# Kernel optimization log

Measured on AMD Instinct MI355X. Metric: run time of the kernel, lower is better.

## Reference

```python
import jax, jax.numpy as jnp
import numpy as np

B, D, R = 16384, 4096, 64       # batch tokens, embed_dim, low_rank_dimension
N_PART = 8                       # number of subspace partitions
P = R // N_PART                  # partition size = 8
N_SEL = 4                        # partitions selected per example


def setup_inputs() -> dict:
    key = jax.random.key(0)
    k1, k2, k3, k4 = jax.random.split(key, 4)
    base = jax.random.normal(k1, (B, D), dtype=jnp.float32)
    source = jax.random.normal(k2, (B, D), dtype=jnp.float32)
    # orthogonal low-rank rotation (torch.nn.utils.parametrizations.orthogonal)
    W, _ = jnp.linalg.qr(jax.random.normal(k3, (D, R), dtype=jnp.float32))  # [D, R], orthonormal cols
    subspaces = jax.random.randint(k4, (B, N_SEL), 0, N_PART)               # partition ids per example
    return {"base": base, "source": source, "W": W, "subspaces": subspaces}


def reference(base, source, W, subspaces):
    # rotate into low-rank space: [B, R]
    rotated_base = base @ W
    rotated_source = source @ W
    diff = rotated_source - rotated_base

    # per-example selected rotated-space indices (contiguous partitions of size P)
    # idx[b] = concat over selected partitions of [p*P, p*P+P)
    idx = (subspaces[:, :, None] * P + jnp.arange(P)).reshape(B, N_SEL * P)  # [B, N_SEL*P]

    # Selecting columns of diff and matching rows of W.T, then matmul, is
    # equivalent to masking unselected rotated dims to zero and doing one GEMM.
    mask = jnp.zeros((B, R), dtype=diff.dtype).at[jnp.arange(B)[:, None], idx].set(1.0)
    output = base + (diff * mask) @ W.T  # [B, D]
    return output.astype(base.dtype)
```

## Files before the change

kernel.cpp:

```cpp
#include <hip/hip_runtime.h>


#define D_DIM 4096
#define R_DIM 64
#define BM    32
#define WAVESTG 16384
#define OFF_RM  65536
#define SMEM_BYTES 70144

typedef short bf16vec8 __attribute__((ext_vector_type(8)));
typedef float f32x4v  __attribute__((ext_vector_type(4)));

#define VMWAIT(N)                                              \
  do {                                                         \
    asm volatile("s_waitcnt vmcnt(" #N ")" ::: "memory");      \
    __builtin_amdgcn_sched_barrier(0);                         \
  } while (0)

__device__ __forceinline__ unsigned int f2bf_u(float f) {
  unsigned int u = __builtin_bit_cast(unsigned int, f);
  return (u + 0x7fffu + ((u >> 16) & 1u)) >> 16;
}
__device__ __forceinline__ unsigned int pack2bf(float a, float b) {
  return f2bf_u(a) | (f2bf_u(b) << 16);
}
__device__ __forceinline__ void async_ld16(const void* g, void* l) {
  __builtin_amdgcn_global_load_lds(
      (const __attribute__((address_space(1))) void*)g,
      (__attribute__((address_space(3))) void*)l, 16, 0, 0);
}

__global__ __launch_bounds__(256)
void lrri_prep(const float* __restrict__ W, unsigned short* __restrict__ Wt,
               unsigned short* __restrict__ Wb) {
  const int idx = blockIdx.x * blockDim.x + threadIdx.x;
  const int k = idx >> 4;
  const int j = (idx & 15) * 4;
  float4 w = *(const float4*)(W + (size_t)k * R_DIM + j);
  ushort4 p;
  p.x = (unsigned short)f2bf_u(w.x);
  p.y = (unsigned short)f2bf_u(w.y);
  p.z = (unsigned short)f2bf_u(w.z);
  p.w = (unsigned short)f2bf_u(w.w);
  *(ushort4*)(Wb + (size_t)k * R_DIM + j) = p;
  Wt[(size_t)(j + 0) * D_DIM + k] = p.x;
  Wt[(size_t)(j + 1) * D_DIM + k] = p.y;
  Wt[(size_t)(j + 2) * D_DIM + k] = p.z;
  Wt[(size_t)(j + 3) * D_DIM + k] = p.w;
}

template<bool USE_WS>
__global__ __launch_bounds__(256, 2)
void lrri_fused(const float* __restrict__ base, const float* __restrict__ srcp,
                const float* __restrict__ W, const int* __restrict__ subs,
                const unsigned short* __restrict__ Wt_bf,
                const unsigned short* __restrict__ Wb_bf,
                float* __restrict__ out)
{
  __shared__ __align__(16) unsigned char smem[SMEM_BYTES];
  const int tid  = threadIdx.x;
  const int wave = tid >> 6;
  const int lane = tid & 63;
  const int l4   = lane & 15;
  const int g    = lane >> 4;
  const int rh   = wave >> 1;
  const int kh   = wave & 1;
  const long rowbase = (long)blockIdx.x * BM;
  const long rowg    = rowbase + rh * 16;
  unsigned char* wbuf = smem + wave * WAVESTG;
  const int off1 = (blockIdx.x * 7) & 63;
  const int off2 = (blockIdx.x * 5) & 15;

  f32x4v acc[4];
  #pragma unroll
  for (int t = 0; t < 4; ++t) acc[t] = (f32x4v){0.f, 0.f, 0.f, 0.f};

  auto stage = [&](int c) {
    const int ch = (c + off1) & 63;
    unsigned char* buf = wbuf + (c & 1) * 8192;
    const long colf = kh * 2048 + ch * 32;
    #pragma unroll
    for (int q = 0; q < 2; ++q) {
      const int r = q * 8 + (lane >> 3);
      const unsigned b = ((unsigned)((lane & 7) * 16)) ^ ((unsigned)(r & 7) << 4);
      const long goff = (rowg + r) * (long)D_DIM + colf + (b >> 2);
      async_ld16(base + goff, buf + q * 1024);
    }
    #pragma unroll
    for (int q = 0; q < 2; ++q) {
      const int r = q * 8 + (lane >> 3);
      const unsigned b = ((unsigned)((lane & 7) * 16)) ^ ((unsigned)(r & 7) << 4);
      const long goff = (rowg + r) * (long)D_DIM + colf + (b >> 2);
      async_ld16(srcp + goff, buf + 2048 + q * 1024);
    }
    #pragma unroll
    for (int q = 0; q < 4; ++q) {
      const int j = q * 16 + (lane >> 2);
      const unsigned kb = ((unsigned)((lane & 3) * 16)) ^ ((unsigned)(j & 3) << 4);
      const char* src = (const char*)Wt_bf + (size_t)j * (D_DIM * 2) +
                        colf * 2 + kb;
      async_ld16(src, buf + 4096 + q * 1024);
    }
  };

  auto compute = [&](int c) {
    const unsigned char* buf = wbuf + (c & 1) * 8192;
    const unsigned sw = (unsigned)((l4 & 7) << 4);
    const unsigned c0 = ((unsigned)(g * 32)) ^ sw;
    const unsigned c1 = ((unsigned)(g * 32 + 16)) ^ sw;
    float4 fb0 = *(const float4*)(buf + l4 * 128 + c0);
    float4 fb1 = *(const float4*)(buf + l4 * 128 + c1);
    float4 fs0 = *(const float4*)(buf + 2048 + l4 * 128 + c0);
    float4 fs1 = *(const float4*)(buf + 2048 + l4 * 128 + c1);
    uint4 af;
    af.x = pack2bf(fs0.x - fb0.x, fs0.y - fb0.y);
    af.y = pack2bf(fs0.z - fb0.z, fs0.w - fb0.w);
    af.z = pack2bf(fs1.x - fb1.x, fs1.y - fb1.y);
    af.w = pack2bf(fs1.z - fb1.z, fs1.w - fb1.w);
    const unsigned wsl = ((unsigned)(g * 16)) ^ ((unsigned)(l4 & 3) << 4);
    #pragma unroll
    for (int t = 0; t < 4; ++t) {
      uint4 wf = *(const uint4*)(buf + 4096 + (t * 16 + l4) * 64 + wsl);
      acc[t] = __builtin_amdgcn_mfma_f32_16x16x32_bf16(
          __builtin_bit_cast(bf16vec8, af),
          __builtin_bit_cast(bf16vec8, wf), acc[t], 0, 0, 0);
    }
  };

  if constexpr (USE_WS) {
    stage(0); stage(1);
    #pragma unroll 1
    for (int c = 0; c < 62; ++c) {
      VMWAIT(8);
      compute(c);
      __builtin_amdgcn_sched_barrier(0);
      stage(c + 2);
    }
    VMWAIT(8);
    compute(62);
    VMWAIT(0);
    compute(63);
  } else {
    #pragma unroll 1
    for (int c = 0; c < 64; ++c) {
      const int ch = (c + off1) & 63;
      unsigned char* buf = wbuf + (c & 1) * 8192;
      const long colf = kh * 2048 + ch * 32;
      #pragma unroll
      for (int q = 0; q < 2; ++q) {
        const int r = q * 8 + (lane >> 3);
        const unsigned b = ((unsigned)((lane & 7) * 16)) ^ ((unsigned)(r & 7) << 4);
        const long goff = (rowg + r) * (long)D_DIM + colf + (b >> 2);
        async_ld16(base + goff, buf + q * 1024);
        async_ld16(srcp + goff, buf + 2048 + q * 1024);
      }
      VMWAIT(0);
      const unsigned sw = (unsigned)((l4 & 7) << 4);
      const unsigned c0 = ((unsigned)(g * 32)) ^ sw;
      const unsigned c1 = ((unsigned)(g * 32 + 16)) ^ sw;
      float4 fb0 = *(const float4*)(buf + l4 * 128 + c0);
      float4 fb1 = *(const float4*)(buf + l4 * 128 + c1);
      float4 fs0 = *(const float4*)(buf + 2048 + l4 * 128 + c0);
      float4 fs1 = *(const float4*)(buf + 2048 + l4 * 128 + c1);
      uint4 af;
      af.x = pack2bf(fs0.x - fb0.x, fs0.y - fb0.y);
      af.y = pack2bf(fs0.z - fb0.z, fs0.w - fb0.w);
      af.z = pack2bf(fs1.x - fb1.x, fs1.y - fb1.y);
      af.w = pack2bf(fs1.z - fb1.z, fs1.w - fb1.w);
      #pragma unroll
      for (int t = 0; t < 4; ++t) {
        unsigned int pq[4];
        #pragma unroll
        for (int e2 = 0; e2 < 4; ++e2) {
          float wa = W[(size_t)(colf + g * 8 + e2 * 2    ) * R_DIM + t * 16 + l4];
          float wb = W[(size_t)(colf + g * 8 + e2 * 2 + 1) * R_DIM + t * 16 + l4];
          pq[e2] = pack2bf(wa, wb);
        }
        uint4 wf; wf.x = pq[0]; wf.y = pq[1]; wf.z = pq[2]; wf.w = pq[3];
        acc[t] = __builtin_amdgcn_mfma_f32_16x16x32_bf16(
            __builtin_bit_cast(bf16vec8, af),
            __builtin_bit_cast(bf16vec8, wf), acc[t], 0, 0, 0);
      }
    }
  }

  {
    float* part = (float*)wbuf;
    #pragma unroll
    for (int t = 0; t < 4; ++t)
      #pragma unroll
      for (int i = 0; i < 4; ++i)
        part[(g * 4 + i) * 72 + t * 16 + l4] = acc[t][i];
  }
  __syncthreads();

  {
    const int row = tid >> 3, jg = tid & 7;
    const int lr  = row & 15;
    const float* pa = (const float*)(smem + ((row >> 4) * 2 + 0) * WAVESTG);
    const float* pb = (const float*)(smem + ((row >> 4) * 2 + 1) * WAVESTG);
    int4 sb = *(const int4*)(subs + (rowbase + row) * 4);
    unsigned mbits = (1u << sb.x) | (1u << sb.y) | (1u << sb.z) | (1u << sb.w);
    unsigned short v[8];
    #pragma unroll
    for (int jj = 0; jj < 8; ++jj) {
      const int j = jg * 8 + jj;
      float sum = pa[lr * 72 + j] + pb[lr * 72 + j];
      v[jj] = ((mbits >> (j >> 3)) & 1u) ? (unsigned short)f2bf_u(sum)
                                         : (unsigned short)0;
    }
    uint4 pk;
    pk.x = (unsigned)v[0] | ((unsigned)v[1] << 16);
    pk.y = (unsigned)v[2] | ((unsigned)v[3] << 16);
    pk.z = (unsigned)v[4] | ((unsigned)v[5] << 16);
    pk.w = (unsigned)v[6] | ((unsigned)v[7] << 16);
    *(uint4*)(smem + OFF_RM + row * 144 + jg * 16) = pk;
  }
  __syncthreads();

  uint4 a2[2][2];
  #pragma unroll
  for (int m = 0; m < 2; ++m)
    #pragma unroll
    for (int s = 0; s < 2; ++s)
      a2[m][s] = *(const uint4*)(smem + OFF_RM + (m * 16 + l4) * 144 +
                                 s * 64 + g * 16);
  float* cbuf = (float*)wbuf;
  #pragma unroll 1
  for (int grp = 0; grp < 16; ++grp) {
    const int ga = (grp + off2) & 15;
    const int cbase = wave * 1024 + ga * 64;
    float4 bb[8];
    #pragma unroll
    for (int v2 = 0; v2 < 8; ++v2) {
      const int r = g + v2 * 4;
      bb[v2] = *(const float4*)(base + (rowbase + r) * D_DIM + cbase + l4 * 4);
    }
    f32x4v a[2][4];
    #pragma unroll
    for (int m = 0; m < 2; ++m)
      #pragma unroll
      for (int t = 0; t < 4; ++t) a[m][t] = (f32x4v){0.f, 0.f, 0.f, 0.f};
    #pragma unroll
    for (int t = 0; t < 4; ++t) {
      #pragma unroll
      for (int s = 0; s < 2; ++s) {
        uint4 bfrag;
        if (USE_WS) {
          bfrag = *(const uint4*)(Wb_bf + (size_t)(cbase + t * 16 + l4) * R_DIM +
                                  s * 32 + g * 8);
        } else {
          const float* wp = W + (size_t)(cbase + t * 16 + l4) * R_DIM + s * 32 + g * 8;
          float4 wa = *(const float4*)(wp);
          float4 wb2 = *(const float4*)(wp + 4);
          bfrag.x = pack2bf(wa.x, wa.y); bfrag.y = pack2bf(wa.z, wa.w);
          bfrag.z = pack2bf(wb2.x, wb2.y); bfrag.w = pack2bf(wb2.z, wb2.w);
        }
        #pragma unroll
        for (int m = 0; m < 2; ++m)
          a[m][t] = __builtin_amdgcn_mfma_f32_16x16x32_bf16(
              __builtin_bit_cast(bf16vec8, a2[m][s]),
              __builtin_bit_cast(bf16vec8, bfrag), a[m][t], 0, 0, 0);
      }
    }
    #pragma unroll
    for (int m = 0; m < 2; ++m)
      #pragma unroll
      for (int t = 0; t < 4; ++t)
        #pragma unroll
        for (int i = 0; i < 4; ++i)
          cbuf[(m * 16 + g * 4 + i) * 72 + t * 16 + l4] = a[m][t][i];
    #pragma unroll
    for (int v2 = 0; v2 < 8; ++v2) {
      const int r = g + v2 * 4;
      f32x4v cv = *(const f32x4v*)(cbuf + r * 72 + l4 * 4);
      float4 o;
      o.x = cv[0] + bb[v2].x;
      o.y = cv[1] + bb[v2].y;
      o.z = cv[2] + bb[v2].z;
      o.w = cv[3] + bb[v2].w;
      *(float4*)(out + (rowbase + r) * D_DIM + cbase + l4 * 4) = o;
    }
  }
}

extern "C" void kernel_launch(void* const* d_in, const int* in_sizes, int n_in,
                              void* d_out, int out_size, void* d_ws, size_t ws_size,
                              hipStream_t stream) {
  const float* base = (const float*)d_in[0];
  const float* srcp = (const float*)d_in[1];
  const float* W    = (const float*)d_in[2];
  const int*   subs = (const int*)d_in[3];
  float* out = (float*)d_out;

  const int nblocks = 16384 / BM;
  const size_t wbytes = (size_t)2 * R_DIM * D_DIM * sizeof(unsigned short);
  if (d_ws && ws_size >= wbytes) {
    unsigned short* Wt = (unsigned short*)d_ws;
    unsigned short* Wb = Wt + (size_t)R_DIM * D_DIM;
    lrri_prep<<<256, 256, 0, stream>>>(W, Wt, Wb);
    lrri_fused<true><<<nblocks, 256, 0, stream>>>(base, srcp, W, subs, Wt, Wb, out);
  } else {
    lrri_fused<false><<<nblocks, 256, 0, stream>>>(base, srcp, W, subs, nullptr, nullptr, out);
  }
}
```

Measured before the change: 227.2 us.

## Split fused kernel into rotate-diff and apply kernels via workspace intermediate

Splits the fused kernel in two. The first kernel computes the masked rotated difference and writes it to workspace as bf16. The second kernel reads it back and applies the up-projection plus the base add, using less shared memory and allowing higher occupancy. This lets each phase run with its own resource limits. In exchange it adds a kernel launch, a global round trip for the intermediate, and extra block-level barriers in the apply loop.

```diff
diff --git a/kernel.cpp b/kernel.cpp
--- a/kernel.cpp
+++ b/kernel.cpp
@@ -5,8 +5,9 @@
 #define R_DIM 64
 #define BM    32
 #define WAVESTG 16384
+#define K1_SMEM 65536
 #define OFF_RM  65536
-#define SMEM_BYTES 70144
+#define FUSED_SMEM 70144
 
 typedef short bf16vec8 __attribute__((ext_vector_type(8)));
 typedef float f32x4v  __attribute__((ext_vector_type(4)));
@@ -49,15 +50,13 @@
   Wt[(size_t)(j + 3) * D_DIM + k] = p.w;
 }
 
-template<bool USE_WS>
 __global__ __launch_bounds__(256, 2)
-void lrri_fused(const float* __restrict__ base, const float* __restrict__ srcp,
-                const float* __restrict__ W, const int* __restrict__ subs,
+void k1_rotdiff(const float* __restrict__ base, const float* __restrict__ srcp,
+                const int* __restrict__ subs,
                 const unsigned short* __restrict__ Wt_bf,
-                const unsigned short* __restrict__ Wb_bf,
-                float* __restrict__ out)
+                unsigned short* __restrict__ rm_g)
 {
-  __shared__ __align__(16) unsigned char smem[SMEM_BYTES];
+  __shared__ __align__(16) unsigned char smem[K1_SMEM];
   const int tid  = threadIdx.x;
   const int wave = tid >> 6;
   const int lane = tid & 63;
@@ -69,7 +68,6 @@
   const long rowg    = rowbase + rh * 16;
   unsigned char* wbuf = smem + wave * WAVESTG;
   const int off1 = (blockIdx.x * 7) & 63;
-  const int off2 = (blockIdx.x * 5) & 15;
 
   f32x4v acc[4];
   #pragma unroll
@@ -127,60 +125,190 @@
     }
   };
 
-  if constexpr (USE_WS) {
-    stage(0); stage(1);
-    #pragma unroll 1
-    for (int c = 0; c < 62; ++c) {
-      VMWAIT(8);
-      compute(c);
-      __builtin_amdgcn_sched_barrier(0);
-      stage(c + 2);
-    }
+  stage(0); stage(1);
+  #pragma unroll 1
+  for (int c = 0; c < 62; ++c) {
     VMWAIT(8);
-    compute(62);
+    compute(c);
+    __builtin_amdgcn_sched_barrier(0);
+    stage(c + 2);
+  }
+  VMWAIT(8);
+  compute(62);
+  VMWAIT(0);
+  compute(63);
+
+  {
+    float* part = (float*)wbuf;
+    #pragma unroll
+    for (int t = 0; t < 4; ++t)
+      #pragma unroll
+      for (int i = 0; i < 4; ++i)
+        part[(g * 4 + i) * 72 + t * 16 + l4] = acc[t][i];
+  }
+  __syncthreads();
+
+  {
+    const int row = tid >> 3, jg = tid & 7;
+    const int lr  = row & 15;
+    const float* pa = (const float*)(smem + ((row >> 4) * 2 + 0) * WAVESTG);
+    const float* pb = (const float*)(smem + ((row >> 4) * 2 + 1) * WAVESTG);
+    int4 sb = *(const int4*)(subs + (rowbase + row) * 4);
+    unsigned mbits = (1u << sb.x) | (1u << sb.y) | (1u << sb.z) | (1u << sb.w);
+    unsigned short v[8];
+    #pragma unroll
+    for (int jj = 0; jj < 8; ++jj) {
+      const int j = jg * 8 + jj;
+      float sum = pa[lr * 72 + j] + pb[lr * 72 + j];
+      v[jj] = ((mbits >> (j >> 3)) & 1u) ? (unsigned short)f2bf_u(sum)
+                                         : (unsigned short)0;
+    }
+    uint4 pk;
+    pk.x = (unsigned)v[0] | ((unsigned)v[1] << 16);
+    pk.y = (unsigned)v[2] | ((unsigned)v[3] << 16);
+    pk.z = (unsigned)v[4] | ((unsigned)v[5] << 16);
+    pk.w = (unsigned)v[6] | ((unsigned)v[7] << 16);
+    *(uint4*)(rm_g + (rowbase + row) * 64 + jg * 8) = pk;
+  }
+}
+
+__global__ __launch_bounds__(256, 4)
+void k2_apply(const float* __restrict__ base,
+              const unsigned short* __restrict__ rm_g,
+              const unsigned short* __restrict__ Wb_bf,
+              float* __restrict__ out)
+{
+  __shared__ __align__(16) unsigned char smem[36864];
+  const int tid  = threadIdx.x;
+  const int wave = tid >> 6;
+  const int lane = tid & 63;
+  const int l4   = lane & 15;
+  const int g    = lane >> 4;
+  const long rowbase = (long)blockIdx.x * BM;
+  const int off2 = (blockIdx.x * 5) & 15;
+
+  uint4 a2[2][2];
+  #pragma unroll
+  for (int m = 0; m < 2; ++m)
+    #pragma unroll
+    for (int s = 0; s < 2; ++s)
+      a2[m][s] = *(const uint4*)(rm_g + (rowbase + m * 16 + l4) * 64 +
+                                 s * 32 + g * 8);
+
+  float* cbuf = (float*)(smem + wave * 9216);
+  #pragma unroll 1
+  for (int grp = 0; grp < 16; ++grp) {
+    const int ga = (grp + off2) & 15;
+    const int cbase = wave * 1024 + ga * 64;
+    float4 bb[8];
+    #pragma unroll
+    for (int v2 = 0; v2 < 8; ++v2) {
+      const int r = g + v2 * 4;
+      bb[v2] = *(const float4*)(base + (rowbase + r) * D_DIM + cbase + l4 * 4);
+    }
+    f32x4v a[2][4];
+    #pragma unroll
+    for (int m = 0; m < 2; ++m)
+      #pragma unroll
+      for (int t = 0; t < 4; ++t) a[m][t] = (f32x4v){0.f, 0.f, 0.f, 0.f};
+    #pragma unroll
+    for (int t = 0; t < 4; ++t) {
+      #pragma unroll
+      for (int s = 0; s < 2; ++s) {
+        uint4 bfrag = *(const uint4*)(Wb_bf +
+            (size_t)(cbase + t * 16 + l4) * R_DIM + s * 32 + g * 8);
+        #pragma unroll
+        for (int m = 0; m < 2; ++m)
+          a[m][t] = __builtin_amdgcn_mfma_f32_16x16x32_bf16(
+              __builtin_bit_cast(bf16vec8, a2[m][s]),
+              __builtin_bit_cast(bf16vec8, bfrag), a[m][t], 0, 0, 0);
+      }
+    }
+    #pragma unroll
+    for (int m = 0; m < 2; ++m)
+      #pragma unroll
+      for (int t = 0; t < 4; ++t)
+        #pragma unroll
+        for (int i = 0; i < 4; ++i)
+          cbuf[(m * 16 + g * 4 + i) * 72 + t * 16 + l4] = a[m][t][i];
+    __syncthreads();
+    #pragma unroll
+    for (int v2 = 0; v2 < 8; ++v2) {
+      const int r = g + v2 * 4;
+      f32x4v cv = *(const f32x4v*)(cbuf + r * 72 + l4 * 4);
+      float4 o;
+      o.x = cv[0] + bb[v2].x;
+      o.y = cv[1] + bb[v2].y;
+      o.z = cv[2] + bb[v2].z;
+      o.w = cv[3] + bb[v2].w;
+      *(float4*)(out + (rowbase + r) * D_DIM + cbase + l4 * 4) = o;
+    }
+    __syncthreads();
+  }
+}
+
+__global__ __launch_bounds__(256, 2)
+void lrri_fused_nows(const float* __restrict__ base, const float* __restrict__ srcp,
+                     const float* __restrict__ W, const int* __restrict__ subs,
+                     float* __restrict__ out)
+{
+  __shared__ __align__(16) unsigned char smem[FUSED_SMEM];
+  const int tid  = threadIdx.x;
+  const int wave = tid >> 6;
+  const int lane = tid & 63;
+  const int l4   = lane & 15;
+  const int g    = lane >> 4;
+  const int rh   = wave >> 1;
+  const int kh   = wave & 1;
+  const long rowbase = (long)blockIdx.x * BM;
+  const long rowg    = rowbase + rh * 16;
+  unsigned char* wbuf = smem + wave * WAVESTG;
+  const int off1 = (blockIdx.x * 7) & 63;
+  const int off2 = (blockIdx.x * 5) & 15;
+
+  f32x4v acc[4];
+  #pragma unroll
+  for (int t = 0; t < 4; ++t) acc[t] = (f32x4v){0.f, 0.f, 0.f, 0.f};
+
+  #pragma unroll 1
+  for (int c = 0; c < 64; ++c) {
+    const int ch = (c + off1) & 63;
+    unsigned char* buf = wbuf + (c & 1) * 8192;
+    const long colf = kh * 2048 + ch * 32;
+    #pragma unroll
+    for (int q = 0; q < 2; ++q) {
+      const int r = q * 8 + (lane >> 3);
+      const unsigned b = ((unsigned)((lane & 7) * 16)) ^ ((unsigned)(r & 7) << 4);
+      const long goff = (rowg + r) * (long)D_DIM + colf + (b >> 2);
+      async_ld16(base + goff, buf + q * 1024);
+      async_ld16(srcp + goff, buf + 2048 + q * 1024);
+    }
     VMWAIT(0);
-    compute(63);
-  } else {
-    #pragma unroll 1
-    for (int c = 0; c < 64; ++c) {
-      const int ch = (c + off1) & 63;
-      unsigned char* buf = wbuf + (c & 1) * 8192;
-      const long colf = kh * 2048 + ch * 32;
-      #pragma unroll
-      for (int q = 0; q < 2; ++q) {
-        const int r = q * 8 + (lane >> 3);
-        const unsigned b = ((unsigned)((lane & 7) * 16)) ^ ((unsigned)(r & 7) << 4);
-        const long goff = (rowg + r) * (long)D_DIM + colf + (b >> 2);
-        async_ld16(base + goff, buf + q * 1024);
-        async_ld16(srcp + goff, buf + 2048 + q * 1024);
+    const unsigned sw = (unsigned)((l4 & 7) << 4);
+    const unsigned c0 = ((unsigned)(g * 32)) ^ sw;
+    const unsigned c1 = ((unsigned)(g * 32 + 16)) ^ sw;
+    float4 fb0 = *(const float4*)(buf + l4 * 128 + c0);
+    float4 fb1 = *(const float4*)(buf + l4 * 128 + c1);
+    float4 fs0 = *(const float4*)(buf + 2048 + l4 * 128 + c0);
+    float4 fs1 = *(const float4*)(buf + 2048 + l4 * 128 + c1);
+    uint4 af;
+    af.x = pack2bf(fs0.x - fb0.x, fs0.y - fb0.y);
+    af.y = pack2bf(fs0.z - fb0.z, fs0.w - fb0.w);
+    af.z = pack2bf(fs1.x - fb1.x, fs1.y - fb1.y);
+    af.w = pack2bf(fs1.z - fb1.z, fs1.w - fb1.w);
+    #pragma unroll
+    for (int t = 0; t < 4; ++t) {
+      unsigned int pq[4];
+      #pragma unroll
+      for (int e2 = 0; e2 < 4; ++e2) {
+        float wa = W[(size_t)(colf + g * 8 + e2 * 2    ) * R_DIM + t * 16 + l4];
+        float wb = W[(size_t)(colf + g * 8 + e2 * 2 + 1) * R_DIM + t * 16 + l4];
+        pq[e2] = pack2bf(wa, wb);
       }
-      VMWAIT(0);
-      const unsigned sw = (unsigned)((l4 & 7) << 4);
-      const unsigned c0 = ((unsigned)(g * 32)) ^ sw;
-      const unsigned c1 = ((unsigned)(g * 32 + 16)) ^ sw;
-      float4 fb0 = *(const float4*)(buf + l4 * 128 + c0);
-      float4 fb1 = *(const float4*)(buf + l4 * 128 + c1);
-      float4 fs0 = *(const float4*)(buf + 2048 + l4 * 128 + c0);
-      float4 fs1 = *(const float4*)(buf + 2048 + l4 * 128 + c1);
-      uint4 af;
-      af.x = pack2bf(fs0.x - fb0.x, fs0.y - fb0.y);
-      af.y = pack2bf(fs0.z - fb0.z, fs0.w - fb0.w);
-      af.z = pack2bf(fs1.x - fb1.x, fs1.y - fb1.y);
-      af.w = pack2bf(fs1.z - fb1.z, fs1.w - fb1.w);
-      #pragma unroll
-      for (int t = 0; t < 4; ++t) {
-        unsigned int pq[4];
-        #pragma unroll
-        for (int e2 = 0; e2 < 4; ++e2) {
-          float wa = W[(size_t)(colf + g * 8 + e2 * 2    ) * R_DIM + t * 16 + l4];
-          float wb = W[(size_t)(colf + g * 8 + e2 * 2 + 1) * R_DIM + t * 16 + l4];
-          pq[e2] = pack2bf(wa, wb);
-        }
-        uint4 wf; wf.x = pq[0]; wf.y = pq[1]; wf.z = pq[2]; wf.w = pq[3];
-        acc[t] = __builtin_amdgcn_mfma_f32_16x16x32_bf16(
-            __builtin_bit_cast(bf16vec8, af),
-            __builtin_bit_cast(bf16vec8, wf), acc[t], 0, 0, 0);
-      }
+      uint4 wf; wf.x = pq[0]; wf.y = pq[1]; wf.z = pq[2]; wf.w = pq[3];
+      acc[t] = __builtin_amdgcn_mfma_f32_16x16x32_bf16(
+          __builtin_bit_cast(bf16vec8, af),
+          __builtin_bit_cast(bf16vec8, wf), acc[t], 0, 0, 0);
     }
   }
 
@@ -245,17 +373,12 @@
     for (int t = 0; t < 4; ++t) {
       #pragma unroll
       for (int s = 0; s < 2; ++s) {
+        const float* wp = W + (size_t)(cbase + t * 16 + l4) * R_DIM + s * 32 + g * 8;
+        float4 wa = *(const float4*)(wp);
+        float4 wb2 = *(const float4*)(wp + 4);
         uint4 bfrag;
-        if (USE_WS) {
-          bfrag = *(const uint4*)(Wb_bf + (size_t)(cbase + t * 16 + l4) * R_DIM +
-                                  s * 32 + g * 8);
-        } else {
-          const float* wp = W + (size_t)(cbase + t * 16 + l4) * R_DIM + s * 32 + g * 8;
-          float4 wa = *(const float4*)(wp);
-          float4 wb2 = *(const float4*)(wp + 4);
-          bfrag.x = pack2bf(wa.x, wa.y); bfrag.y = pack2bf(wa.z, wa.w);
-          bfrag.z = pack2bf(wb2.x, wb2.y); bfrag.w = pack2bf(wb2.z, wb2.w);
-        }
+        bfrag.x = pack2bf(wa.x, wa.y); bfrag.y = pack2bf(wa.z, wa.w);
+        bfrag.z = pack2bf(wb2.x, wb2.y); bfrag.w = pack2bf(wb2.z, wb2.w);
         #pragma unroll
         for (int m = 0; m < 2; ++m)
           a[m][t] = __builtin_amdgcn_mfma_f32_16x16x32_bf16(
@@ -294,13 +417,16 @@
   float* out = (float*)d_out;
 
   const int nblocks = 16384 / BM;
-  const size_t wbytes = (size_t)2 * R_DIM * D_DIM * sizeof(unsigned short);
-  if (d_ws && ws_size >= wbytes) {
+  const size_t wconv = (size_t)2 * R_DIM * D_DIM * sizeof(unsigned short);
+  const size_t rmsz  = (size_t)16384 * R_DIM * sizeof(unsigned short);
+  if (d_ws && ws_size >= wconv + rmsz) {
     unsigned short* Wt = (unsigned short*)d_ws;
     unsigned short* Wb = Wt + (size_t)R_DIM * D_DIM;
+    unsigned short* rm = Wb + (size_t)R_DIM * D_DIM;
     lrri_prep<<<256, 256, 0, stream>>>(W, Wt, Wb);
-    lrri_fused<true><<<nblocks, 256, 0, stream>>>(base, srcp, W, subs, Wt, Wb, out);
+    k1_rotdiff<<<nblocks, 256, 0, stream>>>(base, srcp, subs, Wt, rm);
+    k2_apply<<<nblocks, 256, 0, stream>>>(base, rm, Wb, out);
   } else {
-    lrri_fused<false><<<nblocks, 256, 0, stream>>>(base, srcp, W, subs, nullptr, nullptr, out);
-  }
-}
+    lrri_fused_nows<<<nblocks, 256, 0, stream>>>(base, srcp, W, subs, out);
+  }
+}
```

After: 240.1 us. 1.06x slower.
